# Performance work log

Measured on AMD Instinct MI355X. Metric: run time of the kernel, lower is better.

Reference implementation:

```python
import jax, jax.numpy as jnp
import numpy as np

N_NODES = 163840
N_EDGES = 2621440
F_IN = 64
F_HID = 64
SUBG = 20  # size_subgraph_samples
NEG_SLOPE = 0.2


def gat_conv(x, src, dst, W, a_src, a_dst, b):
    """PyG GATConv, heads=1, concat. src/dst already include self-loops."""
    n = x.shape[0]
    h = x @ W                               # [N, H]
    al_s = h @ a_src                        # [N]
    al_d = h @ a_dst                        # [N]
    e = jax.nn.leaky_relu(al_s[src] + al_d[dst], NEG_SLOPE)  # [E]
    # softmax over incoming edges of each dst node
    m = jax.ops.segment_max(e, dst, num_segments=n)
    ex = jnp.exp(e - m[dst])
    denom = jax.ops.segment_sum(ex, dst, num_segments=n)
    alpha = ex / (denom[dst] + 1e-16)
    msg = h[src] * alpha[:, None]           # [E, H]
    out = jax.ops.segment_sum(msg, dst, num_segments=n)
    return out + b


def setup_inputs() -> dict:
    key = jax.random.key(0)
    ks = jax.random.split(key, 12)
    s = 0.05
    return {
        "x": jax.random.normal(ks[0], (N_NODES, F_IN), jnp.float32),
        "edge_index": jax.random.randint(ks[1], (2, N_EDGES), 0, N_NODES, jnp.int64 if jax.config.jax_enable_x64 else jnp.int32),
        "W1": jax.random.normal(ks[2], (F_IN, F_HID), jnp.float32) * s,
        "a_src1": jax.random.normal(ks[3], (F_HID,), jnp.float32) * s,
        "a_dst1": jax.random.normal(ks[4], (F_HID,), jnp.float32) * s,
        "b1": jnp.zeros((F_HID,), jnp.float32),
        "W2": jax.random.normal(ks[5], (F_HID, F_HID), jnp.float32) * s,
        "a_src2": jax.random.normal(ks[6], (F_HID,), jnp.float32) * s,
        "a_dst2": jax.random.normal(ks[7], (F_HID,), jnp.float32) * s,
        "b2": jnp.zeros((F_HID,), jnp.float32),
        "W_out": jax.random.normal(ks[8], (F_HID * SUBG, 1), jnp.float32) * s,
        "b_out": jnp.zeros((1,), jnp.float32),
    }


def reference(x, edge_index, W1, a_src1, a_dst1, b1, W2, a_src2, a_dst2, b2, W_out, b_out):
    n = x.shape[0]
    loop = jnp.arange(n, dtype=edge_index.dtype)
    src = jnp.concatenate([edge_index[0], loop])  # add_self_loops=True
    dst = jnp.concatenate([edge_index[1], loop])
    h = gat_conv(x, src, dst, W1, a_src1, a_dst1, b1)
    h = jax.nn.relu(h)  # dropout is identity in eval mode
    h = gat_conv(h, src, dst, W2, a_src2, a_dst2, b2)
    h = jax.nn.relu(h)
    h = h.reshape(n // SUBG, F_HID * SUBG)
    return h @ W_out + b_out
```

## Files before the change

### kernel.cpp

```cpp
#include <hip/hip_runtime.h>
#include <math.h>

#define F 64
#define NPB 160
#define STAGE_CAP 6304

typedef __attribute__((ext_vector_type(8))) short bf16x8;
typedef __attribute__((ext_vector_type(4))) float f32x4;

__device__ inline unsigned short f2bf(float f) {
  unsigned int u = __float_as_uint(f);
  u += 0x7fffu + ((u >> 16) & 1u);
  return (unsigned short)(u >> 16);
}


__global__ __launch_bounds__(256) void k_bin_count(const int* __restrict__ edst, int* __restrict__ cntT,
                                                   int e, int ch, int nblk, int nb,
                                                   const float* __restrict__ W1, const float* __restrict__ W2,
                                                   uint4* __restrict__ wf) {
  __shared__ int h[1024];
  int k = blockIdx.x, tid = threadIdx.x;
  if (k == nblk) {
    for (int i = tid; i < 1024; i += 256) {
      int layer = i >> 9, rem = i & 511;
      int cb = rem >> 6, lane = rem & 63;
      int c = cb >> 1, kk = cb & 1;
      int l15 = lane & 15, quad = lane >> 4;
      const float* W = layer ? W2 : W1;
      unsigned short p[8];
      #pragma unroll
      for (int j = 0; j < 8; j++) {
        int kd = kk * 32 + quad * 8 + j;
        p[j] = f2bf(W[kd * F + c * 16 + l15]);
      }
      wf[i] = *(const uint4*)p;
    }
    return;
  }
  for (int i = tid; i < nb; i += 256) h[i] = 0;
  __syncthreads();
  int beg = k * ch, end = min(e, beg + ch);
  for (int i = beg + tid; i < end; i += 256) atomicAdd(&h[edst[i] / NPB], 1);
  __syncthreads();
  for (int b = tid; b < nb; b += 256) cntT[b * nblk + k] = h[b];
}

__global__ __launch_bounds__(256) void k_scan1(const int* __restrict__ counts, int* __restrict__ offs,
                                               int* __restrict__ bsums, int n) {
  int tid = threadIdx.x, lane = tid & 63, wv = tid >> 6;
  int i = blockIdx.x * 256 + tid;
  int v = (i < n) ? counts[i] : 0;
  int x = v;
  #pragma unroll
  for (int o = 1; o <= 32; o <<= 1) { int y = __shfl_up(x, o); if (lane >= o) x += y; }
  __shared__ int wsum[4];
  if (lane == 63) wsum[wv] = x;
  __syncthreads();
  int add = 0;
  for (int w = 0; w < wv; w++) add += wsum[w];
  int incl = x + add;
  if (i < n) offs[i] = incl - v;
  if (tid == 255) bsums[blockIdx.x] = incl;
}

__global__ __launch_bounds__(256) void k_scan2(int* __restrict__ bs, int nb,
                                               float* __restrict__ out, const float* __restrict__ bo, int ng) {
  __shared__ int wsum[4];
  __shared__ int carry_sh;
  int tid = threadIdx.x, lane = tid & 63, wv = tid >> 6;
  float b0 = bo[0];
  for (int i = tid; i < ng; i += 256) out[i] = b0;
  if (tid == 0) carry_sh = 0;
  __syncthreads();
  for (int base = 0; base < nb; base += 256) {
    int i = base + tid;
    int v = (i < nb) ? bs[i] : 0;
    int x = v;
    #pragma unroll
    for (int o = 1; o <= 32; o <<= 1) { int y = __shfl_up(x, o); if (lane >= o) x += y; }
    if (lane == 63) wsum[wv] = x;
    __syncthreads();
    int add = 0;
    for (int w = 0; w < wv; w++) add += wsum[w];
    int incl = x + add;
    int carry = carry_sh;
    if (i < nb) bs[i] = incl - v + carry;
    __syncthreads();
    if (tid == 255) carry_sh = carry + incl;
    __syncthreads();
  }
}

template<bool IN_BF16>
__device__ __forceinline__ void gemm_body(const void* __restrict__ in, const uint4* __restrict__ wf,
                                          const float* __restrict__ avs, const float* __restrict__ avd,
                                          unsigned short* __restrict__ hgb, float* __restrict__ als,
                                          float* __restrict__ ald, int n, int bid, int nbl) {
  int tid = threadIdx.x, lane = tid & 63, wv = tid >> 6;
  int l15 = lane & 15, quad = lane >> 4;
  bf16x8 bfr[4][2];
  #pragma unroll
  for (int cb = 0; cb < 8; cb++) {
    uint4 u = wf[cb * 64 + lane];
    bfr[cb >> 1][cb & 1] = *(const bf16x8*)&u;
  }
  float as_l[4], ad_l[4];
  #pragma unroll
  for (int c = 0; c < 4; c++) { as_l[c] = avs[c * 16 + l15]; ad_l[c] = avd[c * 16 + l15]; }

  int nchunks = n >> 6;
  for (int chunk = bid; chunk < nchunks; chunk += nbl) {
    int r0 = (chunk << 6) + (wv << 4);
    bf16x8 a0, a1;
    if constexpr (IN_BF16) {
      const uint4* row4 = (const uint4*)((const unsigned short*)in + (size_t)(r0 + l15) * F);
      uint4 u0 = row4[quad];
      uint4 u1 = row4[quad + 4];
      a0 = *(const bf16x8*)&u0;
      a1 = *(const bf16x8*)&u1;
    } else {
      const float4* xr = (const float4*)((const float*)in + (size_t)(r0 + l15) * F + quad * 8);
      float4 xa = xr[0], xb = xr[1];
      float4 xc = xr[8], xd = xr[9];
      a0[0] = (short)f2bf(xa.x); a0[1] = (short)f2bf(xa.y); a0[2] = (short)f2bf(xa.z); a0[3] = (short)f2bf(xa.w);
      a0[4] = (short)f2bf(xb.x); a0[5] = (short)f2bf(xb.y); a0[6] = (short)f2bf(xb.z); a0[7] = (short)f2bf(xb.w);
      a1[0] = (short)f2bf(xc.x); a1[1] = (short)f2bf(xc.y); a1[2] = (short)f2bf(xc.z); a1[3] = (short)f2bf(xc.w);
      a1[4] = (short)f2bf(xd.x); a1[5] = (short)f2bf(xd.y); a1[6] = (short)f2bf(xd.z); a1[7] = (short)f2bf(xd.w);
    }
    f32x4 cfr[4];
    #pragma unroll
    for (int c = 0; c < 4; c++) {
      cfr[c] = (f32x4){0.f, 0.f, 0.f, 0.f};
      cfr[c] = __builtin_amdgcn_mfma_f32_16x16x32_bf16(a0, bfr[c][0], cfr[c], 0, 0, 0);
      cfr[c] = __builtin_amdgcn_mfma_f32_16x16x32_bf16(a1, bfr[c][1], cfr[c], 0, 0, 0);
    }
    #pragma unroll
    for (int i = 0; i < 4; i++) {
      int row = r0 + quad * 4 + i;
      #pragma unroll
      for (int c = 0; c < 4; c++) hgb[(size_t)row * F + c * 16 + l15] = f2bf(cfr[c][i]);
      float ps = cfr[0][i] * as_l[0] + cfr[1][i] * as_l[1] + cfr[2][i] * as_l[2] + cfr[3][i] * as_l[3];
      float pd = cfr[0][i] * ad_l[0] + cfr[1][i] * ad_l[1] + cfr[2][i] * ad_l[2] + cfr[3][i] * ad_l[3];
      #pragma unroll
      for (int o = 1; o <= 8; o <<= 1) { ps += __shfl_xor(ps, o); pd += __shfl_xor(pd, o); }
      if (l15 == 0) { als[row] = ps; ald[row] = pd; }
    }
  }
}

__global__ __launch_bounds__(256) void k_scatter_gemm1(const int* __restrict__ esrc, const int* __restrict__ edst,
                                                       const int* __restrict__ posT, const int* __restrict__ bsums,
                                                       unsigned int* __restrict__ binned,
                                                       int e, int ch, int nblk, int nb,
                                                       const float* __restrict__ x, const uint4* __restrict__ wf,
                                                       const float* __restrict__ avs, const float* __restrict__ avd,
                                                       unsigned short* __restrict__ hgb, float* __restrict__ als,
                                                       float* __restrict__ ald, int n) {
  int k = blockIdx.x, tid = threadIdx.x;
  if (k < nblk) {
    __shared__ int cur[1024];
    for (int b = tid; b < nb; b += 256) {
      int idx = b * nblk + k;
      cur[b] = posT[idx] + bsums[idx >> 8];
    }
    __syncthreads();
    int beg = k * ch, end = min(e, beg + ch);
    for (int i = beg + tid; i < end; i += 256) {
      int d = edst[i];
      int b = d / NPB;
      unsigned int ld = (unsigned int)(d - b * NPB);
      int p = atomicAdd(&cur[b], 1);
      binned[p] = (unsigned int)esrc[i] | (ld << 24);
    }
    return;
  }
  gemm_body<false>(x, wf, avs, avd, hgb, als, ald, n, k - nblk, (int)gridDim.x - nblk);
}

__global__ __launch_bounds__(256) void k_gemm2(const unsigned short* __restrict__ in, const uint4* __restrict__ wf,
                                               const float* __restrict__ avs, const float* __restrict__ avd,
                                               unsigned short* __restrict__ hgb, float* __restrict__ als,
                                               float* __restrict__ ald, int n) {
  gemm_body<true>(in, wf, avs, avd, hgb, als, ald, n, blockIdx.x, gridDim.x);
}

__global__ __launch_bounds__(256) void k_bucket_csr(const unsigned int* __restrict__ binned,
                                                    const int* __restrict__ posT, const int* __restrict__ bsums,
                                                    int* __restrict__ ssrc, int* __restrict__ offs,
                                                    int n, int nblk, int nb, int e) {
  __shared__ int ncnt[NPB];
  __shared__ int noff[NPB];
  __shared__ int cur[NPB];
  __shared__ int sc[256];
  __shared__ int stage[STAGE_CAP];
  int b = blockIdx.x, tid = threadIdx.x;
  int node0 = b * NPB;
  int nn = min(NPB, n - node0);
  int i0 = b * nblk;
  int ebeg = posT[i0] + bsums[i0 >> 8];
  int eend;
  if (b == nb - 1) eend = e;
  else { int i1 = (b + 1) * nblk; eend = posT[i1] + bsums[i1 >> 8]; }
  int ecnt = eend - ebeg;
  for (int i = tid; i < NPB; i += 256) ncnt[i] = 0;
  __syncthreads();
  for (int i = tid; i < ecnt; i += 256) { unsigned int v = binned[ebeg + i]; atomicAdd(&ncnt[v >> 24], 1); }
  __syncthreads();
  int x = (tid < nn) ? ncnt[tid] + 1 : 0;
  sc[tid] = x;
  __syncthreads();
  #pragma unroll
  for (int o = 1; o < 256; o <<= 1) {
    int y = (tid >= o) ? sc[tid - o] : 0;
    __syncthreads();
    sc[tid] += y;
    __syncthreads();
  }
  if (tid < nn) noff[tid] = sc[tid] - x;
  __syncthreads();
  int tot = ecnt + nn;
  int outbase = ebeg + node0;
  bool staged = (tot <= STAGE_CAP);
  if (tid < nn) {
    cur[tid] = noff[tid] + 1;
    offs[node0 + tid] = outbase + noff[tid];
    if (staged) stage[noff[tid]] = node0 + tid;
    else        ssrc[outbase + noff[tid]] = node0 + tid;
  }
  __syncthreads();
  if (staged) {
    for (int i = tid; i < ecnt; i += 256) {
      unsigned int v = binned[ebeg + i];
      int p = atomicAdd(&cur[v >> 24], 1);
      stage[p] = (int)(v & 0xFFFFFFu);
    }
    __syncthreads();
    for (int i = tid; i < tot; i += 256) ssrc[outbase + i] = stage[i];
  } else {
    for (int i = tid; i < ecnt; i += 256) {
      unsigned int v = binned[ebeg + i];
      int p = atomicAdd(&cur[v >> 24], 1);
      ssrc[outbase + p] = (int)(v & 0xFFFFFFu);
    }
  }
  if (b == 0 && tid == 0) offs[n] = e + n;
}

template<int MODE>
__global__ __launch_bounds__(256) void k_spmm(const int* __restrict__ offs, const int* __restrict__ ssrc,
                                              const unsigned short* __restrict__ hgb,
                                              const float* __restrict__ als, const float* __restrict__ ald,
                                              const float* __restrict__ bias, const float* __restrict__ Wout,
                                              void* __restrict__ outp, int n) {
  int tid = threadIdx.x, lane = tid & 63, wv = tid >> 6;
  int g8 = lane >> 3, l8 = lane & 7;
  const uint4* hg4 = (const uint4*)hgb;
  float4 bl0 = ((const float4*)bias)[l8 * 2];
  float4 bl1 = ((const float4*)bias)[l8 * 2 + 1];

  __shared__ float gsl[3];
  if (MODE == 1 && tid < 3) gsl[tid] = 0.f;

  int node = (blockIdx.x * 4 + wv) * 8 + g8;
  int cnode = min(node, n - 1);
  bool nodeok = node < n;
  int beg = offs[cnode];
  int deg = nodeok ? (offs[cnode + 1] - beg) : 0;
  int degc = max(deg - 1, 0);
  float aldv = ald[cnode];

  int dm = deg;
  #pragma unroll
  for (int o = 8; o <= 32; o <<= 1) dm = max(dm, __shfl_xor(dm, o));

  float s = 0.f;
  float acc[8];
  #pragma unroll
  for (int k = 0; k < 8; k++) acc[k] = 0.f;

  #pragma unroll 2
  for (int j = 0; j < dm; j++) {
    int jj = min(j, degc);
    int src = ssrc[beg + jj];
    float t = als[src] + aldv;
    t = fmaxf(t, 0.2f * t);
    float ex = (j < deg) ? __expf(t) : 0.f;
    s += ex;
    uint4 u = hg4[(size_t)src * 8 + l8];
    acc[0] = fmaf(ex, __uint_as_float(u.x << 16), acc[0]);
    acc[1] = fmaf(ex, __uint_as_float(u.x & 0xffff0000u), acc[1]);
    acc[2] = fmaf(ex, __uint_as_float(u.y << 16), acc[2]);
    acc[3] = fmaf(ex, __uint_as_float(u.y & 0xffff0000u), acc[3]);
    acc[4] = fmaf(ex, __uint_as_float(u.z << 16), acc[4]);
    acc[5] = fmaf(ex, __uint_as_float(u.z & 0xffff0000u), acc[5]);
    acc[6] = fmaf(ex, __uint_as_float(u.w << 16), acc[6]);
    acc[7] = fmaf(ex, __uint_as_float(u.w & 0xffff0000u), acc[7]);
  }

  float iv = 1.f / (s + 1e-16f);
  float r[8];
  r[0] = fmaxf(fmaf(acc[0], iv, bl0.x), 0.f);
  r[1] = fmaxf(fmaf(acc[1], iv, bl0.y), 0.f);
  r[2] = fmaxf(fmaf(acc[2], iv, bl0.z), 0.f);
  r[3] = fmaxf(fmaf(acc[3], iv, bl0.w), 0.f);
  r[4] = fmaxf(fmaf(acc[4], iv, bl1.x), 0.f);
  r[5] = fmaxf(fmaf(acc[5], iv, bl1.y), 0.f);
  r[6] = fmaxf(fmaf(acc[6], iv, bl1.z), 0.f);
  r[7] = fmaxf(fmaf(acc[7], iv, bl1.w), 0.f);

  if constexpr (MODE == 0) {
    if (!nodeok) return;
    unsigned short p[8];
    #pragma unroll
    for (int k = 0; k < 8; k++) p[k] = f2bf(r[k]);
    ((uint4*)outp)[(size_t)node * 8 + l8] = *(const uint4*)p;
  } else {
    int node0 = blockIdx.x * 32;
    int grp0 = node0 / 20;
    int grp = cnode / 20, slot = cnode - grp * 20;
    const float* wr = Wout + slot * F + l8 * 8;
    float dot = 0.f;
    #pragma unroll
    for (int k = 0; k < 8; k++) dot = fmaf(r[k], wr[k], dot);
    #pragma unroll
    for (int o = 1; o <= 4; o <<= 1) dot += __shfl_xor(dot, o);
    __syncthreads();
    if (nodeok && l8 == 0) atomicAdd(&gsl[grp - grp0], dot);
    __syncthreads();
    if (tid < 3) {
      float v = gsl[tid];
      if (v != 0.f) atomicAdd((float*)outp + grp0 + tid, v);
    }
  }
}

extern "C" void kernel_launch(void* const* d_in, const int* in_sizes, int n_in,
                              void* d_out, int out_size, void* d_ws, size_t ws_size,
                              hipStream_t stream) {
  const float* x   = (const float*)d_in[0];
  const int*   ei  = (const int*)d_in[1];
  const float* W1  = (const float*)d_in[2];
  const float* as1 = (const float*)d_in[3];
  const float* ad1 = (const float*)d_in[4];
  const float* b1  = (const float*)d_in[5];
  const float* W2  = (const float*)d_in[6];
  const float* as2 = (const float*)d_in[7];
  const float* ad2 = (const float*)d_in[8];
  const float* b2  = (const float*)d_in[9];
  const float* Wo  = (const float*)d_in[10];
  const float* bo  = (const float*)d_in[11];
  float* out = (float*)d_out;

  const int N = in_sizes[0] / F;
  const int E = in_sizes[1] / 2;
  const int* esrc = ei;
  const int* edst = ei + E;

  size_t off = 0;
  auto alloc = [&](size_t bytes) -> void* {
    void* p = (char*)d_ws + off;
    off += (bytes + 255) & ~(size_t)255;
    return p;
  };
  float* A    = (float*)alloc((size_t)N * F * 4);
  unsigned short* hgb = (unsigned short*)alloc((size_t)N * F * 2);
  float* als  = (float*)alloc((size_t)N * 4);
  float* ald  = (float*)alloc((size_t)N * 4);
  int* offs   = (int*)alloc((size_t)(N + 1) * 4);
  int* bsums  = (int*)alloc(8192);
  int* ssrc   = (int*)alloc((size_t)(E + N) * 4);
  uint4* wf   = (uint4*)alloc(16384);
  (void)ws_size; (void)n_in; (void)out_size;

  const int NBLK = 256;
  const int NB = (N + NPB - 1) / NPB;
  const int CH = (E + NBLK - 1) / NBLK;
  const int FLAT = NB * NBLK;

  int* cntT = (int*)A;
  int* posT = (int*)((char*)A + ((size_t)FLAT * 4 + 1024));
  unsigned int* binned = (unsigned int*)((char*)A + (size_t)8 * 1024 * 1024);

  int gF = (FLAT + 255) / 256;
  int NG = N / 20;

  k_bin_count<<<NBLK + 1, 256, 0, stream>>>(edst, cntT, E, CH, NBLK, NB, W1, W2, wf);
  k_scan1<<<gF, 256, 0, stream>>>(cntT, posT, bsums, FLAT);
  k_scan2<<<1, 256, 0, stream>>>(bsums, gF, out, bo, NG);
  k_scatter_gemm1<<<NBLK + (N >> 6), 256, 0, stream>>>(esrc, edst, posT, bsums, binned, E, CH, NBLK, NB,
                                                       x, wf, as1, ad1, hgb, als, ald, N);
  k_bucket_csr<<<NB, 256, 0, stream>>>(binned, posT, bsums, ssrc, offs, N, NBLK, NB, E);

  int gSp = (N + 31) / 32;
  k_spmm<0><<<gSp, 256, 0, stream>>>(offs, ssrc, hgb, als, ald, b1, nullptr, A, N);
  k_gemm2<<<(N >> 6), 256, 0, stream>>>((const unsigned short*)A, wf + 512, as2, ad2, hgb, als, ald, N);
  k_spmm<1><<<gSp, 256, 0, stream>>>(offs, ssrc, hgb, als, ald, b2, Wo, out, N);
}
```

Before: 321.3 us.

## Replace global count-scan binning with fixed-capacity buckets and atomic reservation

```diff
diff --git a/kernel.cpp b/kernel.cpp
--- a/kernel.cpp
+++ b/kernel.cpp
@@ -4,6 +4,7 @@
 #define F 64
 #define NPB 160
 #define STAGE_CAP 6304
+#define BCAP 3584
 
 typedef __attribute__((ext_vector_type(8))) short bf16x8;
 typedef __attribute__((ext_vector_type(4))) float f32x4;
@@ -14,14 +15,11 @@
   return (unsigned short)(u >> 16);
 }
 
-
-__global__ __launch_bounds__(256) void k_bin_count(const int* __restrict__ edst, int* __restrict__ cntT,
-                                                   int e, int ch, int nblk, int nb,
-                                                   const float* __restrict__ W1, const float* __restrict__ W2,
-                                                   uint4* __restrict__ wf) {
-  __shared__ int h[1024];
-  int k = blockIdx.x, tid = threadIdx.x;
-  if (k == nblk) {
+__global__ __launch_bounds__(256) void k_prep(const float* __restrict__ W1, const float* __restrict__ W2,
+                                              uint4* __restrict__ wf, int* __restrict__ bcnt, int nb,
+                                              float* __restrict__ out, const float* __restrict__ bo, int ng) {
+  int tid = threadIdx.x;
+  if (blockIdx.x == 0) {
     for (int i = tid; i < 1024; i += 256) {
       int layer = i >> 9, rem = i & 511;
       int cb = rem >> 6, lane = rem & 63;
@@ -36,59 +34,10 @@
       }
       wf[i] = *(const uint4*)p;
     }
-    return;
-  }
-  for (int i = tid; i < nb; i += 256) h[i] = 0;
-  __syncthreads();
-  int beg = k * ch, end = min(e, beg + ch);
-  for (int i = beg + tid; i < end; i += 256) atomicAdd(&h[edst[i] / NPB], 1);
-  __syncthreads();
-  for (int b = tid; b < nb; b += 256) cntT[b * nblk + k] = h[b];
-}
-
-__global__ __launch_bounds__(256) void k_scan1(const int* __restrict__ counts, int* __restrict__ offs,
-                                               int* __restrict__ bsums, int n) {
-  int tid = threadIdx.x, lane = tid & 63, wv = tid >> 6;
-  int i = blockIdx.x * 256 + tid;
-  int v = (i < n) ? counts[i] : 0;
-  int x = v;
-  #pragma unroll
-  for (int o = 1; o <= 32; o <<= 1) { int y = __shfl_up(x, o); if (lane >= o) x += y; }
-  __shared__ int wsum[4];
-  if (lane == 63) wsum[wv] = x;
-  __syncthreads();
-  int add = 0;
-  for (int w = 0; w < wv; w++) add += wsum[w];
-  int incl = x + add;
-  if (i < n) offs[i] = incl - v;
-  if (tid == 255) bsums[blockIdx.x] = incl;
-}
-
-__global__ __launch_bounds__(256) void k_scan2(int* __restrict__ bs, int nb,
-                                               float* __restrict__ out, const float* __restrict__ bo, int ng) {
-  __shared__ int wsum[4];
-  __shared__ int carry_sh;
-  int tid = threadIdx.x, lane = tid & 63, wv = tid >> 6;
-  float b0 = bo[0];
-  for (int i = tid; i < ng; i += 256) out[i] = b0;
-  if (tid == 0) carry_sh = 0;
-  __syncthreads();
-  for (int base = 0; base < nb; base += 256) {
-    int i = base + tid;
-    int v = (i < nb) ? bs[i] : 0;
-    int x = v;
-    #pragma unroll
-    for (int o = 1; o <= 32; o <<= 1) { int y = __shfl_up(x, o); if (lane >= o) x += y; }
-    if (lane == 63) wsum[wv] = x;
-    __syncthreads();
-    int add = 0;
-    for (int w = 0; w < wv; w++) add += wsum[w];
-    int incl = x + add;
-    int carry = carry_sh;
-    if (i < nb) bs[i] = incl - v + carry;
-    __syncthreads();
-    if (tid == 255) carry_sh = carry + incl;
-    __syncthreads();
+  } else {
+    for (int i = tid; i < nb * 16; i += 256) bcnt[i] = 0;
+    float b0 = bo[0];
+    for (int i = tid; i < ng; i += 256) out[i] = b0;
   }
 }
 
@@ -150,45 +99,97 @@
 }
 
 __global__ __launch_bounds__(256) void k_scatter_gemm1(const int* __restrict__ esrc, const int* __restrict__ edst,
-                                                       const int* __restrict__ posT, const int* __restrict__ bsums,
-                                                       unsigned int* __restrict__ binned,
-                                                       int e, int ch, int nblk, int nb,
+                                                       int* __restrict__ bcnt, unsigned int* __restrict__ binned,
+                                                       int e, int ch, int S,
                                                        const float* __restrict__ x, const uint4* __restrict__ wf,
                                                        const float* __restrict__ avs, const float* __restrict__ avd,
                                                        unsigned short* __restrict__ hgb, float* __restrict__ als,
                                                        float* __restrict__ ald, int n) {
   int k = blockIdx.x, tid = threadIdx.x;
-  if (k < nblk) {
+  if (k < S) {
+    __shared__ int hist[1024];
     __shared__ int cur[1024];
-    for (int b = tid; b < nb; b += 256) {
-      int idx = b * nblk + k;
-      cur[b] = posT[idx] + bsums[idx >> 8];
-    }
+    for (int i = tid; i < 1024; i += 256) hist[i] = 0;
     __syncthreads();
     int beg = k * ch, end = min(e, beg + ch);
-    for (int i = beg + tid; i < end; i += 256) {
+    int len = end - beg;
+    if (len <= 0) return;
+    int nv = len >> 2;
+    for (int g = tid; g < nv; g += 256) {
+      int4 d4 = *(const int4*)(edst + beg + (g << 2));
+      atomicAdd(&hist[d4.x / NPB], 1);
+      atomicAdd(&hist[d4.y / NPB], 1);
+      atomicAdd(&hist[d4.z / NPB], 1);
+      atomicAdd(&hist[d4.w / NPB], 1);
+    }
+    for (int i = beg + (nv << 2) + tid; i < end; i += 256) atomicAdd(&hist[edst[i] / NPB], 1);
+    __syncthreads();
+    for (int b = tid; b < 1024; b += 256) {
+      int c = hist[b];
+      int base = 0;
+      if (c) base = atomicAdd(&bcnt[b * 16], c);
+      cur[b] = b * BCAP + base;
+    }
+    __syncthreads();
+    for (int g = tid; g < nv; g += 256) {
+      int i = beg + (g << 2);
+      int4 d4 = *(const int4*)(edst + i);
+      int4 s4 = *(const int4*)(esrc + i);
+      #pragma unroll
+      for (int j = 0; j < 4; j++) {
+        int d = (j == 0) ? d4.x : (j == 1) ? d4.y : (j == 2) ? d4.z : d4.w;
+        int s = (j == 0) ? s4.x : (j == 1) ? s4.y : (j == 2) ? s4.z : s4.w;
+        int b = d / NPB;
+        int p = atomicAdd(&cur[b], 1);
+        if (p < (b + 1) * BCAP) binned[p] = (unsigned int)s | ((unsigned int)(d - b * NPB) << 24);
+      }
+    }
+    for (int i = beg + (nv << 2) + tid; i < end; i += 256) {
       int d = edst[i];
       int b = d / NPB;
-      unsigned int ld = (unsigned int)(d - b * NPB);
       int p = atomicAdd(&cur[b], 1);
-      binned[p] = (unsigned int)esrc[i] | (ld << 24);
+      if (p < (b + 1) * BCAP) binned[p] = (unsigned int)esrc[i] | ((unsigned int)(d - b * NPB) << 24);
     }
     return;
   }
-  gemm_body<false>(x, wf, avs, avd, hgb, als, ald, n, k - nblk, (int)gridDim.x - nblk);
-}
-
-__global__ __launch_bounds__(256) void k_gemm2(const unsigned short* __restrict__ in, const uint4* __restrict__ wf,
-                                               const float* __restrict__ avs, const float* __restrict__ avd,
-                                               unsigned short* __restrict__ hgb, float* __restrict__ als,
-                                               float* __restrict__ ald, int n) {
-  gemm_body<true>(in, wf, avs, avd, hgb, als, ald, n, blockIdx.x, gridDim.x);
+  gemm_body<false>(x, wf, avs, avd, hgb, als, ald, n, k - S, (int)gridDim.x - S);
+}
+
+__global__ __launch_bounds__(256) void k_bucket_scan(const int* __restrict__ bcnt, int* __restrict__ obase,
+                                                     int* __restrict__ offs, int n, int nb) {
+  __shared__ int wsum[4];
+  __shared__ int carry_sh;
+  int tid = threadIdx.x, lane = tid & 63, wv = tid >> 6;
+  if (tid == 0) carry_sh = 0;
+  __syncthreads();
+  for (int base = 0; base < nb; base += 256) {
+    int b = base + tid;
+    int v = 0;
+    if (b < nb) {
+      int cnt = min(bcnt[b * 16], BCAP);
+      int nn = min(NPB, n - b * NPB);
+      v = cnt + nn;
+    }
+    int x = v;
+    #pragma unroll
+    for (int o = 1; o <= 32; o <<= 1) { int y = __shfl_up(x, o); if (lane >= o) x += y; }
+    if (lane == 63) wsum[wv] = x;
+    __syncthreads();
+    int add = 0;
+    for (int w = 0; w < wv; w++) add += wsum[w];
+    int incl = x + add;
+    int carry = carry_sh;
+    if (b < nb) obase[b] = incl - v + carry;
+    __syncthreads();
+    if (tid == 255) carry_sh = carry + incl;
+    __syncthreads();
+  }
+  if (tid == 0) offs[n] = carry_sh;
 }
 
 __global__ __launch_bounds__(256) void k_bucket_csr(const unsigned int* __restrict__ binned,
-                                                    const int* __restrict__ posT, const int* __restrict__ bsums,
-                                                    int* __restrict__ ssrc, int* __restrict__ offs,
-                                                    int n, int nblk, int nb, int e) {
+                                                    const int* __restrict__ bcnt, const int* __restrict__ obase,
+                                                    int* __restrict__ ssrc, int* __restrict__ offs, int n) {
   __shared__ int ncnt[NPB];
   __shared__ int noff[NPB];
   __shared__ int cur[NPB];
@@ -197,12 +198,9 @@
   int b = blockIdx.x, tid = threadIdx.x;
   int node0 = b * NPB;
   int nn = min(NPB, n - node0);
-  int i0 = b * nblk;
-  int ebeg = posT[i0] + bsums[i0 >> 8];
-  int eend;
-  if (b == nb - 1) eend = e;
-  else { int i1 = (b + 1) * nblk; eend = posT[i1] + bsums[i1 >> 8]; }
-  int ecnt = eend - ebeg;
+  int ebeg = b * BCAP;
+  int ecnt = min(bcnt[b * 16], BCAP);
+  int outbase = obase[b];
   for (int i = tid; i < NPB; i += 256) ncnt[i] = 0;
   __syncthreads();
   for (int i = tid; i < ecnt; i += 256) { unsigned int v = binned[ebeg + i]; atomicAdd(&ncnt[v >> 24], 1); }
@@ -220,7 +218,6 @@
   if (tid < nn) noff[tid] = sc[tid] - x;
   __syncthreads();
   int tot = ecnt + nn;
-  int outbase = ebeg + node0;
   bool staged = (tot <= STAGE_CAP);
   if (tid < nn) {
     cur[tid] = noff[tid] + 1;
@@ -244,7 +241,13 @@
       ssrc[outbase + p] = (int)(v & 0xFFFFFFu);
     }
   }
-  if (b == 0 && tid == 0) offs[n] = e + n;
+}
+
+__global__ __launch_bounds__(256) void k_gemm2(const unsigned short* __restrict__ in, const uint4* __restrict__ wf,
+                                               const float* __restrict__ avs, const float* __restrict__ avd,
+                                               unsigned short* __restrict__ hgb, float* __restrict__ als,
+                                               float* __restrict__ ald, int n) {
+  gemm_body<true>(in, wf, avs, avd, hgb, als, ald, n, blockIdx.x, gridDim.x);
 }
 
 template<int MODE>
@@ -368,29 +371,24 @@
   float* als  = (float*)alloc((size_t)N * 4);
   float* ald  = (float*)alloc((size_t)N * 4);
   int* offs   = (int*)alloc((size_t)(N + 1) * 4);
-  int* bsums  = (int*)alloc(8192);
+  int* bcnt   = (int*)alloc((size_t)1024 * 16 * 4);
+  int* obase  = (int*)alloc((size_t)1024 * 4);
   int* ssrc   = (int*)alloc((size_t)(E + N) * 4);
   uint4* wf   = (uint4*)alloc(16384);
   (void)ws_size; (void)n_in; (void)out_size;
 
-  const int NBLK = 256;
+  const int S = 256;
   const int NB = (N + NPB - 1) / NPB;
-  const int CH = (E + NBLK - 1) / NBLK;
-  const int FLAT = NB * NBLK;
-
-  int* cntT = (int*)A;
-  int* posT = (int*)((char*)A + ((size_t)FLAT * 4 + 1024));
+  const int CH = (((E + S - 1) / S) + 3) & ~3;
+  const int NG = N / 20;
+
   unsigned int* binned = (unsigned int*)((char*)A + (size_t)8 * 1024 * 1024);
 
-  int gF = (FLAT + 255) / 256;
-  int NG = N / 20;
-
-  k_bin_count<<<NBLK + 1, 256, 0, stream>>>(edst, cntT, E, CH, NBLK, NB, W1, W2, wf);
-  k_scan1<<<gF, 256, 0, stream>>>(cntT, posT, bsums, FLAT);
-  k_scan2<<<1, 256, 0, stream>>>(bsums, gF, out, bo, NG);
-  k_scatter_gemm1<<<NBLK + (N >> 6), 256, 0, stream>>>(esrc, edst, posT, bsums, binned, E, CH, NBLK, NB,
-                                                       x, wf, as1, ad1, hgb, als, ald, N);
-  k_bucket_csr<<<NB, 256, 0, stream>>>(binned, posT, bsums, ssrc, offs, N, NBLK, NB, E);
+  k_prep<<<2, 256, 0, stream>>>(W1, W2, wf, bcnt, NB, out, bo, NG);
+  k_scatter_gemm1<<<S + (N >> 6), 256, 0, stream>>>(esrc, edst, bcnt, binned, E, CH, S,
+                                                    x, wf, as1, ad1, hgb, als, ald, N);
+  k_bucket_scan<<<1, 256, 0, stream>>>(bcnt, obase, offs, N, NB);
+  k_bucket_csr<<<NB, 256, 0, stream>>>(binned, bcnt, obase, ssrc, offs, N);
 
   int gSp = (N + 31) / 32;
   k_spmm<0><<<gSp, 256, 0, stream>>>(offs, ssrc, hgb, als, ald, b1, nullptr, A, N);
```

Measured after the change: 295.0 us. 1.09x faster.
